# Kernel optimization log

Measured on AMD Instinct MI355X. Metric: run time of the kernel, lower is better.

## Reference

```python
import jax, jax.numpy as jnp
import numpy as np

B, L, D, H = 4, 4096, 2048, 16
HD = D // H  # head_dim = 128
EPS = 1e-9

def phi(x):
    # ELU(x) + 1 : non-negative feature map
    return jax.nn.elu(x) + 1.0

def setup_inputs() -> dict:
    key = jax.random.key(0)
    k1, k2, k3 = jax.random.split(key, 3)
    x = jax.random.normal(k1, (B, L, D), dtype=jnp.float32)
    W_qkv = jax.random.normal(k2, (3 * D, D), dtype=jnp.float32) * (D ** -0.5)
    W_out = jax.random.normal(k3, (D, D), dtype=jnp.float32) * (D ** -0.5)
    return {"x": x, "W_qkv": W_qkv, "W_out": W_out}

def reference(x, W_qkv, W_out):
    b, l, d = x.shape
    qkv = x @ W_qkv.T                      # (B, L, 3D)
    q, k, v = jnp.split(qkv, 3, axis=-1)   # each (B, L, D)
    # (B, L, H, HD) -> (B, H, L, HD)
    q = q.reshape(b, l, H, HD).transpose(0, 2, 1, 3)
    k = k.reshape(b, l, H, HD).transpose(0, 2, 1, 3)
    v = v.reshape(b, l, H, HD).transpose(0, 2, 1, 3)
    q = phi(q)
    k = phi(k)
    kv_cumsum = jnp.cumsum(k * v, axis=2)  # prefix sum over sequence dim
    k_cumsum = jnp.cumsum(k, axis=2)
    out = q * kv_cumsum / (q * k_cumsum + EPS)
    out = out.transpose(0, 2, 1, 3).reshape(b, l, d)
    return (out @ W_out.T) * (HD ** -0.5)
```

## Files before the change

kernel.cpp:

```cpp
#include <hip/hip_runtime.h>
#include <hip/hip_bf16.h>
#include <stdint.h>

#define B_ 4
#define L_ 4096
#define D_ 2048
#define TD_ (3 * D_)
#define CHUNKS 128
#define CLEN (L_ / CHUNKS)
#define M_ (B_ * L_)
#define K_ 2048
#define NT (K_ / 64)

typedef __bf16 bf16x8 __attribute__((ext_vector_type(8)));
typedef float f32x4 __attribute__((ext_vector_type(4)));
typedef ushort u16x8 __attribute__((ext_vector_type(8)));

__device__ __forceinline__ ushort f2bf(float f) {
  uint32_t u = __builtin_bit_cast(uint32_t, f);
  u += 0x7fffu + ((u >> 16) & 1u);
  return (ushort)(u >> 16);
}

__device__ __forceinline__ float bf2f(ushort u) {
  return __builtin_bit_cast(float, (uint32_t)u << 16);
}

__device__ __forceinline__ float phi_f(float x) {
  return x > 0.f ? x + 1.f : __expf(x);
}

__device__ __forceinline__ void gload_lds16(const ushort* g, ushort* l) {
  __builtin_amdgcn_global_load_lds(
      (__attribute__((address_space(1))) void*)(g),
      (__attribute__((address_space(3))) void*)(l), 16, 0, 0);
}

#define SBAR() __builtin_amdgcn_s_barrier()
#define SCHED0() __builtin_amdgcn_sched_barrier(0)
#define LGKM0() asm volatile("s_waitcnt lgkmcnt(0)" ::: "memory")
#define MFMA16(a, b, c) __builtin_amdgcn_mfma_f32_16x16x32_bf16((a), (b), (c), 0, 0, 0)

__global__ void cvt_bf16_kernel(const float* __restrict__ in,
                                ushort* __restrict__ out, int n4) {
  int i = blockIdx.x * blockDim.x + threadIdx.x;
  if (i >= n4) return;
  float4 v = reinterpret_cast<const float4*>(in)[i];
  ushort4 o;
  o.x = f2bf(v.x); o.y = f2bf(v.y); o.z = f2bf(v.z); o.w = f2bf(v.w);
  reinterpret_cast<ushort4*>(out)[i] = o;
}

__device__ __forceinline__ void stage_half(const ushort* __restrict__ G,
                                           int row0, int k0, char* lds_half,
                                           int tid) {
#pragma unroll
  for (int lp = 0; lp < 2; ++lp) {
    const int p = lp * 8192 + tid * 16;
    const int row = p >> 7;
    const int cb = (p & 127) ^ ((row & 7) << 4);
    gload_lds16(G + (size_t)(row0 + row) * K_ + k0 + (cb >> 1),
                (ushort*)(lds_half + p));
  }
}

__device__ __forceinline__ bf16x8 frag(const char* tile, int row, int cb) {
  return *reinterpret_cast<const bf16x8*>(tile + row * 128 +
                                          (cb ^ ((row & 7) << 4)));
}

#define KTILE(t, c)                                                            \
  {                                                                            \
    const int k0 = (t) * 64;                                                   \
         \
    _Pragma("unroll") for (int i = 0; i < 4; ++i) {                            \
      af[i][0] = frag(lsA##c, wm + i * 16 + l16, kg * 16);                     \
      af[i][1] = frag(lsA##c, wm + i * 16 + l16, 64 + kg * 16);                \
    }                                                                          \
    _Pragma("unroll") for (int j = 0; j < 2; ++j) {                            \
      bfr[j][0] = frag(lsB##c, wn + j * 16 + l16, kg * 16);                    \
      bfr[j][1] = frag(lsB##c, wn + j * 16 + l16, 64 + kg * 16);               \
    }                                                                          \
    if ((t) + 1 < NT) stage_half(A, rA, k0 + 64, lsAo##c, tid);                \
    SCHED0(); SBAR(); LGKM0(); SCHED0();                                       \
    __builtin_amdgcn_s_setprio(1);                                             \
    _Pragma("unroll") for (int i = 0; i < 4; ++i)                              \
    _Pragma("unroll") for (int j = 0; j < 2; ++j)                              \
    _Pragma("unroll") for (int ks = 0; ks < 2; ++ks)                           \
        acc[i][j] = MFMA16(af[i][ks], bfr[j][ks], acc[i][j]);                  \
    __builtin_amdgcn_s_setprio(0); SBAR();                                     \
                          \
    _Pragma("unroll") for (int j = 2; j < 4; ++j) {                            \
      bfr[j][0] = frag(lsB##c, wn + j * 16 + l16, kg * 16);                    \
      bfr[j][1] = frag(lsB##c, wn + j * 16 + l16, 64 + kg * 16);               \
    }                                                                          \
    if ((t) + 1 < NT) stage_half(A, rA + 128, k0 + 64, lsAo##c + 16384, tid);  \
    SCHED0(); SBAR(); LGKM0(); SCHED0();                                       \
    __builtin_amdgcn_s_setprio(1);                                             \
    _Pragma("unroll") for (int i = 0; i < 4; ++i)                              \
    _Pragma("unroll") for (int j = 2; j < 4; ++j)                              \
    _Pragma("unroll") for (int ks = 0; ks < 2; ++ks)                           \
        acc[i][j] = MFMA16(af[i][ks], bfr[j][ks], acc[i][j]);                  \
    __builtin_amdgcn_s_setprio(0); SBAR();                                     \
            \
    _Pragma("unroll") for (int i = 0; i < 4; ++i) {                            \
      af[i][0] = frag(lsA##c, wm + 64 + i * 16 + l16, kg * 16);                \
      af[i][1] = frag(lsA##c, wm + 64 + i * 16 + l16, 64 + kg * 16);           \
    }                                                                          \
    if ((t) + 2 < NT) stage_half(Bm, rB, k0 + 128, lsB##c, tid);               \
    SCHED0(); SBAR(); LGKM0(); SCHED0();                                       \
    __builtin_amdgcn_s_setprio(1);                                             \
    _Pragma("unroll") for (int i = 0; i < 4; ++i)                              \
    _Pragma("unroll") for (int j = 2; j < 4; ++j)                              \
    _Pragma("unroll") for (int ks = 0; ks < 2; ++ks)                           \
        acc[4 + i][j] = MFMA16(af[i][ks], bfr[j][ks], acc[4 + i][j]);          \
    __builtin_amdgcn_s_setprio(0); SBAR();                                     \
                  \
    if ((t) + 2 < NT) {                                                        \
      stage_half(Bm, rB + 128, k0 + 128, lsB##c + 16384, tid);                 \
      SCHED0();                                                                \
      asm volatile("s_waitcnt vmcnt(4)" ::: "memory");                         \
    } else {                                                                   \
      SCHED0();                                                                \
      asm volatile("s_waitcnt vmcnt(0)" ::: "memory");                         \
    }                                                                          \
    SBAR();                                                                    \
    __builtin_amdgcn_s_setprio(1);                                             \
    _Pragma("unroll") for (int i = 0; i < 4; ++i)                              \
    _Pragma("unroll") for (int j = 0; j < 2; ++j)                              \
    _Pragma("unroll") for (int ks = 0; ks < 2; ++ks)                           \
        acc[4 + i][j] = MFMA16(af[i][ks], bfr[j][ks], acc[4 + i][j]);          \
    __builtin_amdgcn_s_setprio(0); SBAR();                                     \
  }

__device__ __forceinline__ void gemm_core(const ushort* __restrict__ A,
                                          const ushort* __restrict__ Bm,
                                          int bm, int bn, char* ls,
                                          f32x4 (&acc)[8][4]) {
  const int tid = threadIdx.x;
  const int lane = tid & 63, wid = tid >> 6;
  const int wm = (wid >> 2) * 128, wn = (wid & 3) * 64;
  const int l16 = lane & 15, kg = lane >> 4;
  const int rA = bm * 256, rB = bn * 256;

  char* lsA0 = ls;
  char* lsA1 = ls + 32768;
  char* lsB0 = ls + 65536;
  char* lsB1 = ls + 98304;
  char* lsAo0 = lsA1;
  char* lsAo1 = lsA0;

  stage_half(A, rA, 0, lsA0, tid);
  stage_half(A, rA + 128, 0, lsA0 + 16384, tid);
  stage_half(Bm, rB, 0, lsB0, tid);
  stage_half(Bm, rB + 128, 0, lsB0 + 16384, tid);
  stage_half(Bm, rB, 64, lsB1, tid);
  stage_half(Bm, rB + 128, 64, lsB1 + 16384, tid);
  asm volatile("s_waitcnt vmcnt(4)" ::: "memory");
  SBAR();

  bf16x8 af[4][2], bfr[4][2];
#pragma unroll 1
  for (int t2 = 0; t2 < NT; t2 += 2) {
    KTILE(t2, 0);
    KTILE(t2 + 1, 1);
  }
}

__global__ __launch_bounds__(512, 2) void gemm_qkv8(
    const ushort* __restrict__ A, const ushort* __restrict__ Bm,
    ushort* __restrict__ qb, ushort* __restrict__ kb, ushort* __restrict__ vb) {
  extern __shared__ char ls[];
  const int nwg = gridDim.x;
  const int wg = blockIdx.x;
  const int swz = (wg & 7) * (nwg >> 3) + (wg >> 3);
  const int MT = M_ / 256;
  const int bm = swz % MT, bn = swz / MT;

  f32x4 acc[8][4] = {};
  gemm_core(A, Bm, bm, bn, ls, acc);

  const int seg = bn >> 3;
  ushort* dst = seg == 0 ? qb : (seg == 1 ? kb : vb);
  const int colbase = bn * 256 - seg * 2048;
  const int tid = threadIdx.x;
  const int lane = tid & 63, wid = tid >> 6;
  const int wm = (wid >> 2) * 128, wn = (wid & 3) * 64;
  const int l16 = lane & 15, kg = lane >> 4;
#pragma unroll
  for (int i = 0; i < 8; ++i) {
    const int row0 = bm * 256 + wm + i * 16 + kg * 4;
#pragma unroll
    for (int j = 0; j < 4; ++j) {
      const int col = colbase + wn + j * 16 + l16;
      ushort* cp = dst + (size_t)row0 * D_ + col;
#pragma unroll
      for (int r = 0; r < 4; ++r) cp[(size_t)r * D_] = f2bf(acc[i][j][r]);
    }
  }
}

__global__ __launch_bounds__(512, 2) void gemm_out8(
    const ushort* __restrict__ A, const ushort* __restrict__ Bm,
    float* __restrict__ C, float scale) {
  extern __shared__ char ls[];
  const int nwg = gridDim.x;
  const int wg = blockIdx.x;
  const int swz = (wg & 7) * (nwg >> 3) + (wg >> 3);
  const int MT = M_ / 256;
  const int bm = swz % MT, bn = swz / MT;

  f32x4 acc[8][4] = {};
  gemm_core(A, Bm, bm, bn, ls, acc);

  const int tid = threadIdx.x;
  const int lane = tid & 63, wid = tid >> 6;
  const int wm = (wid >> 2) * 128, wn = (wid & 3) * 64;
  const int l16 = lane & 15, kg = lane >> 4;
#pragma unroll
  for (int i = 0; i < 8; ++i) {
    const int row0 = bm * 256 + wm + i * 16 + kg * 4;
#pragma unroll
    for (int j = 0; j < 4; ++j) {
      const int col = bn * 256 + wn + j * 16 + l16;
      float* cp = C + (size_t)row0 * D_ + col;
#pragma unroll
      for (int r = 0; r < 4; ++r) cp[(size_t)r * D_] = acc[i][j][r] * scale;
    }
  }
}

__global__ void chunk_sums_kernel(const ushort* __restrict__ kb,
                                  const ushort* __restrict__ vb,
                                  float* __restrict__ sums) {
  const int d0 = threadIdx.x * 8;
  const int b = blockIdx.y, c = blockIdx.z;
  float sk[8] = {}, skv[8] = {};
  const size_t rowbase = (size_t)b * L_ + (size_t)c * CLEN;
  for (int l = 0; l < CLEN; ++l) {
    const size_t idx = (rowbase + l) * D_ + d0;
    u16x8 k8 = *reinterpret_cast<const u16x8*>(kb + idx);
    u16x8 v8 = *reinterpret_cast<const u16x8*>(vb + idx);
#pragma unroll
    for (int j = 0; j < 8; ++j) {
      float k = phi_f(bf2f(k8[j]));
      sk[j] += k;
      skv[j] = fmaf(k, bf2f(v8[j]), skv[j]);
    }
  }
  float* s = sums + ((size_t)(b * CHUNKS + c) * 2) * D_ + d0;
#pragma unroll
  for (int j = 0; j < 8; ++j) {
    s[j] = sk[j];
    s[D_ + j] = skv[j];
  }
}

__global__ void chunk_prefix_kernel(float* __restrict__ sums) {
  const int idx = blockIdx.x * 256 + threadIdx.x;
  const int b = idx >> 11, d = idx & (D_ - 1);
  float rk = 0.f, rkv = 0.f;
  for (int c = 0; c < CHUNKS; ++c) {
    float* s = sums + ((size_t)(b * CHUNKS + c) * 2) * D_ + d;
    float sk = s[0], skv = s[D_];
    s[0] = rk;
    s[D_] = rkv;
    rk += sk;
    rkv += skv;
  }
}

__global__ void apply_kernel(const ushort* __restrict__ qb,
                             const ushort* __restrict__ kb,
                             const ushort* __restrict__ vb,
                             const float* __restrict__ sums,
                             ushort* __restrict__ outb) {
  const int d0 = threadIdx.x * 8;
  const int b = blockIdx.y, c = blockIdx.z;
  const float* s = sums + ((size_t)(b * CHUNKS + c) * 2) * D_ + d0;
  float rk[8], rkv[8];
#pragma unroll
  for (int j = 0; j < 8; ++j) {
    rk[j] = s[j];
    rkv[j] = s[D_ + j];
  }
  const size_t rowbase = (size_t)b * L_ + (size_t)c * CLEN;
  for (int l = 0; l < CLEN; ++l) {
    const size_t idx = (rowbase + l) * D_ + d0;
    u16x8 q8 = *reinterpret_cast<const u16x8*>(qb + idx);
    u16x8 k8 = *reinterpret_cast<const u16x8*>(kb + idx);
    u16x8 v8 = *reinterpret_cast<const u16x8*>(vb + idx);
    u16x8 o8;
#pragma unroll
    for (int j = 0; j < 8; ++j) {
      float q = phi_f(bf2f(q8[j]));
      float k = phi_f(bf2f(k8[j]));
      float v = bf2f(v8[j]);
      rkv[j] = fmaf(k, v, rkv[j]);
      rk[j] += k;
      float o = (q * rkv[j]) / fmaf(q, rk[j], 1e-9f);
      o8[j] = f2bf(o);
    }
    *reinterpret_cast<u16x8*>(outb + idx) = o8;
  }
}

extern "C" void kernel_launch(void* const* d_in, const int* in_sizes, int n_in,
                              void* d_out, int out_size, void* d_ws, size_t ws_size,
                              hipStream_t stream) {
  (void)in_sizes; (void)n_in; (void)out_size; (void)ws_size;
  const float* x = (const float*)d_in[0];
  const float* Wqkv = (const float*)d_in[1];
  const float* Wout = (const float*)d_in[2];
  float* out = (float*)d_out;

  ushort* kb = (ushort*)d_out;
  ushort* vb = kb + (size_t)M_ * D_;

  char* ws = (char*)d_ws;
  size_t off = 0;
  auto alloc = [&](size_t bytes) -> void* {
    off = (off + 255) & ~(size_t)255;
    void* p = ws + off;
    off += bytes;
    return p;
  };
  ushort* qb = (ushort*)alloc((size_t)M_ * D_ * 2);
  ushort* xb = (ushort*)alloc((size_t)M_ * D_ * 2);
  ushort* wqb = (ushort*)alloc((size_t)TD_ * D_ * 2);
  ushort* wob = (ushort*)alloc((size_t)D_ * D_ * 2);
  float* sums = (float*)alloc((size_t)B_ * CHUNKS * 2 * D_ * 4);
  ushort* outb = xb;

  (void)hipFuncSetAttribute((const void*)gemm_qkv8,
                            hipFuncAttributeMaxDynamicSharedMemorySize, 131072);
  (void)hipFuncSetAttribute((const void*)gemm_out8,
                            hipFuncAttributeMaxDynamicSharedMemorySize, 131072);

  cvt_bf16_kernel<<<(M_ * D_ / 4 + 255) / 256, 256, 0, stream>>>(x, xb, M_ * D_ / 4);
  cvt_bf16_kernel<<<(TD_ * D_ / 4 + 255) / 256, 256, 0, stream>>>(Wqkv, wqb, TD_ * D_ / 4);
  cvt_bf16_kernel<<<(D_ * D_ / 4 + 255) / 256, 256, 0, stream>>>(Wout, wob, D_ * D_ / 4);

  gemm_qkv8<<<dim3((TD_ / 256) * (M_ / 256)), 512, 131072, stream>>>(xb, wqb, qb, kb, vb);

  chunk_sums_kernel<<<dim3(1, B_, CHUNKS), 256, 0, stream>>>(kb, vb, sums);
  chunk_prefix_kernel<<<dim3(B_ * D_ / 256), 256, 0, stream>>>(sums);
  apply_kernel<<<dim3(1, B_, CHUNKS), 256, 0, stream>>>(qb, kb, vb, sums, outb);

  gemm_out8<<<dim3((D_ / 256) * (M_ / 256)), 512, 131072, stream>>>(outb, wob, out,
                                                                    0.08838834764831845f);
}
```

Baseline: 626.7 us.

## Prefetch LDS fragments across k-tiles and remap workgroups for XCD-local reuse

Restructures the GEMM inner loop so A/B fragments for the next k-tile are read from LDS during the current tile's last MFMA phase. Fragment registers are split into low/high halves, and the explicit lgkmcnt(0) waits after each barrier are dropped. LDS addresses now come from precomputed swizzled base pointers plus constant offsets, which removes per-load index math. A new workgroup remap groups M-tiles per XCD so neighbouring blocks share A rows in L2. The cost is higher register pressure and reliance on compiler-inserted waits for LDS reads.

```diff
diff --git a/kernel.cpp b/kernel.cpp
--- a/kernel.cpp
+++ b/kernel.cpp
@@ -38,7 +38,6 @@
 
 #define SBAR() __builtin_amdgcn_s_barrier()
 #define SCHED0() __builtin_amdgcn_sched_barrier(0)
-#define LGKM0() asm volatile("s_waitcnt lgkmcnt(0)" ::: "memory")
 #define MFMA16(a, b, c) __builtin_amdgcn_mfma_f32_16x16x32_bf16((a), (b), (c), 0, 0, 0)
 
 __global__ void cvt_bf16_kernel(const float* __restrict__ in,
@@ -64,72 +63,71 @@
   }
 }
 
-__device__ __forceinline__ bf16x8 frag(const char* tile, int row, int cb) {
-  return *reinterpret_cast<const bf16x8*>(tile + row * 128 +
-                                          (cb ^ ((row & 7) << 4)));
-}
-
-#define KTILE(t, c)                                                            \
+#define RD(p, off) (*reinterpret_cast<const bf16x8*>((p) + (off)))
+
+#define KTILE(t, c, o)                                                         \
   {                                                                            \
-    const int k0 = (t) * 64;                                                   \
-         \
-    _Pragma("unroll") for (int i = 0; i < 4; ++i) {                            \
-      af[i][0] = frag(lsA##c, wm + i * 16 + l16, kg * 16);                     \
-      af[i][1] = frag(lsA##c, wm + i * 16 + l16, 64 + kg * 16);                \
+                                                                 \
+    _Pragma("unroll") for (int j = 0; j < 2; ++j) {                            \
+      bfrH[j][0] = RD(pB##c##0, 4096 + j * 2048);                              \
+      bfrH[j][1] = RD(pB##c##1, 4096 + j * 2048);                              \
     }                                                                          \
-    _Pragma("unroll") for (int j = 0; j < 2; ++j) {                            \
-      bfr[j][0] = frag(lsB##c, wn + j * 16 + l16, kg * 16);                    \
-      bfr[j][1] = frag(lsB##c, wn + j * 16 + l16, 64 + kg * 16);               \
-    }                                                                          \
-    if ((t) + 1 < NT) stage_half(A, rA, k0 + 64, lsAo##c, tid);                \
-    SCHED0(); SBAR(); LGKM0(); SCHED0();                                       \
+    if ((t) + 1 < NT) stage_half(A, rA, (t) * 64 + 64, lsA##o, tid);           \
+    SCHED0(); SBAR();                                                          \
     __builtin_amdgcn_s_setprio(1);                                             \
     _Pragma("unroll") for (int i = 0; i < 4; ++i)                              \
     _Pragma("unroll") for (int j = 0; j < 2; ++j)                              \
     _Pragma("unroll") for (int ks = 0; ks < 2; ++ks)                           \
-        acc[i][j] = MFMA16(af[i][ks], bfr[j][ks], acc[i][j]);                  \
+        acc[i][j] = MFMA16(afL[i][ks], bfrL##c[j][ks], acc[i][j]);             \
     __builtin_amdgcn_s_setprio(0); SBAR();                                     \
-                          \
-    _Pragma("unroll") for (int j = 2; j < 4; ++j) {                            \
-      bfr[j][0] = frag(lsB##c, wn + j * 16 + l16, kg * 16);                    \
-      bfr[j][1] = frag(lsB##c, wn + j * 16 + l16, 64 + kg * 16);               \
+                                                                 \
+    _Pragma("unroll") for (int i = 0; i < 4; ++i) {                            \
+      afH[i][0] = RD(pA##c##0, 8192 + i * 2048);                               \
+      afH[i][1] = RD(pA##c##1, 8192 + i * 2048);                               \
     }                                                                          \
-    if ((t) + 1 < NT) stage_half(A, rA + 128, k0 + 64, lsAo##c + 16384, tid);  \
-    SCHED0(); SBAR(); LGKM0(); SCHED0();                                       \
+    if ((t) + 1 < NT) stage_half(A, rA + 128, (t) * 64 + 64,                   \
+                                 lsA##o + 16384, tid);                         \
+    SCHED0(); SBAR();                                                          \
     __builtin_amdgcn_s_setprio(1);                                             \
     _Pragma("unroll") for (int i = 0; i < 4; ++i)                              \
-    _Pragma("unroll") for (int j = 2; j < 4; ++j)                              \
+    _Pragma("unroll") for (int j = 0; j < 2; ++j)                              \
     _Pragma("unroll") for (int ks = 0; ks < 2; ++ks)                           \
-        acc[i][j] = MFMA16(af[i][ks], bfr[j][ks], acc[i][j]);                  \
+        acc[i][2 + j] = MFMA16(afL[i][ks], bfrH[j][ks], acc[i][2 + j]);        \
     __builtin_amdgcn_s_setprio(0); SBAR();                                     \
-            \
-    _Pragma("unroll") for (int i = 0; i < 4; ++i) {                            \
-      af[i][0] = frag(lsA##c, wm + 64 + i * 16 + l16, kg * 16);                \
-      af[i][1] = frag(lsA##c, wm + 64 + i * 16 + l16, 64 + kg * 16);           \
-    }                                                                          \
-    if ((t) + 2 < NT) stage_half(Bm, rB, k0 + 128, lsB##c, tid);               \
-    SCHED0(); SBAR(); LGKM0(); SCHED0();                                       \
+                                                                 \
+    if ((t) + 2 < NT) stage_half(Bm, rB, (t) * 64 + 128, lsB##c, tid);         \
+    SCHED0(); SBAR();                                                          \
     __builtin_amdgcn_s_setprio(1);                                             \
     _Pragma("unroll") for (int i = 0; i < 4; ++i)                              \
-    _Pragma("unroll") for (int j = 2; j < 4; ++j)                              \
+    _Pragma("unroll") for (int j = 0; j < 2; ++j)                              \
     _Pragma("unroll") for (int ks = 0; ks < 2; ++ks)                           \
-        acc[4 + i][j] = MFMA16(af[i][ks], bfr[j][ks], acc[4 + i][j]);          \
+        acc[4 + i][2 + j] = MFMA16(afH[i][ks], bfrH[j][ks], acc[4 + i][2 + j]);\
     __builtin_amdgcn_s_setprio(0); SBAR();                                     \
-                  \
+                                                                 \
     if ((t) + 2 < NT) {                                                        \
-      stage_half(Bm, rB + 128, k0 + 128, lsB##c + 16384, tid);                 \
+      stage_half(Bm, rB + 128, (t) * 64 + 128, lsB##c + 16384, tid);           \
       SCHED0();                                                                \
       asm volatile("s_waitcnt vmcnt(4)" ::: "memory");                         \
     } else {                                                                   \
       SCHED0();                                                                \
       asm volatile("s_waitcnt vmcnt(0)" ::: "memory");                         \
     }                                                                          \
-    SBAR();                                                                    \
+    if ((t) + 1 < NT) {                                                        \
+      _Pragma("unroll") for (int i = 0; i < 4; ++i) {                          \
+        afL[i][0] = RD(pA##o##0, i * 2048);                                    \
+        afL[i][1] = RD(pA##o##1, i * 2048);                                    \
+      }                                                                        \
+      _Pragma("unroll") for (int j = 0; j < 2; ++j) {                          \
+        bfrL##o[j][0] = RD(pB##o##0, j * 2048);                                \
+        bfrL##o[j][1] = RD(pB##o##1, j * 2048);                                \
+      }                                                                        \
+    }                                                                          \
+    SCHED0(); SBAR();                                                          \
     __builtin_amdgcn_s_setprio(1);                                             \
     _Pragma("unroll") for (int i = 0; i < 4; ++i)                              \
     _Pragma("unroll") for (int j = 0; j < 2; ++j)                              \
     _Pragma("unroll") for (int ks = 0; ks < 2; ++ks)                           \
-        acc[4 + i][j] = MFMA16(af[i][ks], bfr[j][ks], acc[4 + i][j]);          \
+        acc[4 + i][j] = MFMA16(afH[i][ks], bfrL##c[j][ks], acc[4 + i][j]);     \
     __builtin_amdgcn_s_setprio(0); SBAR();                                     \
   }
 
@@ -147,8 +145,18 @@
   char* lsA1 = ls + 32768;
   char* lsB0 = ls + 65536;
   char* lsB1 = ls + 98304;
-  char* lsAo0 = lsA1;
-  char* lsAo1 = lsA0;
+
+  const int v7 = l16 & 7;
+  const int aoff0 = 16 * (kg ^ v7);
+  const int aoff1 = 16 * ((4 + kg) ^ v7);
+  const char* pA00 = lsA0 + (wm + l16) * 128 + aoff0;
+  const char* pA01 = lsA0 + (wm + l16) * 128 + aoff1;
+  const char* pA10 = lsA1 + (wm + l16) * 128 + aoff0;
+  const char* pA11 = lsA1 + (wm + l16) * 128 + aoff1;
+  const char* pB00 = lsB0 + (wn + l16) * 128 + aoff0;
+  const char* pB01 = lsB0 + (wn + l16) * 128 + aoff1;
+  const char* pB10 = lsB1 + (wn + l16) * 128 + aoff0;
+  const char* pB11 = lsB1 + (wn + l16) * 128 + aoff1;
 
   stage_half(A, rA, 0, lsA0, tid);
   stage_half(A, rA + 128, 0, lsA0 + 16384, tid);
@@ -159,23 +167,40 @@
   asm volatile("s_waitcnt vmcnt(4)" ::: "memory");
   SBAR();
 
-  bf16x8 af[4][2], bfr[4][2];
+  bf16x8 afL[4][2], afH[4][2], bfrH[2][2], bfrL0[2][2], bfrL1[2][2];
+#pragma unroll
+  for (int i = 0; i < 4; ++i) {
+    afL[i][0] = RD(pA00, i * 2048);
+    afL[i][1] = RD(pA01, i * 2048);
+  }
+#pragma unroll
+  for (int j = 0; j < 2; ++j) {
+    bfrL0[j][0] = RD(pB00, j * 2048);
+    bfrL0[j][1] = RD(pB01, j * 2048);
+  }
+
 #pragma unroll 1
   for (int t2 = 0; t2 < NT; t2 += 2) {
-    KTILE(t2, 0);
-    KTILE(t2 + 1, 1);
-  }
+    KTILE(t2, 0, 1);
+    KTILE(t2 + 1, 1, 0);
+  }
+}
+
+__device__ __forceinline__ void remap(int wg, int BN_TILES, int* bm, int* bn) {
+  const int xcd = wg & 7;
+  const int idx = wg >> 3;
+  const int bi = idx & 3;
+  const int t = idx >> 2;
+  *bn = t % BN_TILES;
+  *bm = xcd * 8 + (t / BN_TILES) * 4 + bi;
 }
 
 __global__ __launch_bounds__(512, 2) void gemm_qkv8(
     const ushort* __restrict__ A, const ushort* __restrict__ Bm,
     ushort* __restrict__ qb, ushort* __restrict__ kb, ushort* __restrict__ vb) {
   extern __shared__ char ls[];
-  const int nwg = gridDim.x;
-  const int wg = blockIdx.x;
-  const int swz = (wg & 7) * (nwg >> 3) + (wg >> 3);
-  const int MT = M_ / 256;
-  const int bm = swz % MT, bn = swz / MT;
+  int bm, bn;
+  remap(blockIdx.x, TD_ / 256, &bm, &bn);
 
   f32x4 acc[8][4] = {};
   gemm_core(A, Bm, bm, bn, ls, acc);
@@ -204,11 +229,8 @@
     const ushort* __restrict__ A, const ushort* __restrict__ Bm,
     float* __restrict__ C, float scale) {
   extern __shared__ char ls[];
-  const int nwg = gridDim.x;
-  const int wg = blockIdx.x;
-  const int swz = (wg & 7) * (nwg >> 3) + (wg >> 3);
-  const int MT = M_ / 256;
-  const int bm = swz % MT, bn = swz / MT;
+  int bm, bn;
+  remap(blockIdx.x, D_ / 256, &bm, &bn);
 
   f32x4 acc[8][4] = {};
   gemm_core(A, Bm, bm, bn, ls, acc);
```

After: 1.160 ms. 85.1% more time.
